# Kernel tuning notes

Measured on AMD Instinct MI355X. Metric: run time of the kernel, lower is better.

Reference implementation:

```python
import jax, jax.numpy as jnp
import numpy as np

N_NODES = 10000
N_EDGES = 80000
IN_DIM = 512
H1, H2, OUT_DIM = 4096, 1024, 7
NEG_SLOPE = 0.2


def _gat_layer(x, src, dst, W, a_src, a_dst, b, n_nodes):
    # x: [N, F_in] -> h: [N, F_out]
    h = x @ W
    # per-edge attention logits: a_src . h_i + a_dst . h_j (PyG GATConv, heads=1)
    e = jax.nn.leaky_relu((h @ a_src)[src] + (h @ a_dst)[dst], NEG_SLOPE)
    # segment softmax over destination nodes
    m = jax.ops.segment_max(e, dst, num_segments=n_nodes)
    ex = jnp.exp(e - m[dst])
    denom = jax.ops.segment_sum(ex, dst, num_segments=n_nodes)
    alpha = ex / denom[dst]
    # scatter-add weighted messages
    out = jax.ops.segment_sum(alpha[:, None] * h[src], dst, num_segments=n_nodes)
    return out + b


def setup_inputs() -> dict:
    key = jax.random.key(0)
    ks = jax.random.split(key, 16)
    s = 0.05
    inp = {
        "x": jax.random.normal(ks[0], (N_NODES, IN_DIM), dtype=jnp.float32),
        "edge_index": jax.random.randint(ks[1], (2, N_EDGES), 0, N_NODES, dtype=jnp.int32),
        "W1": jax.random.normal(ks[2], (IN_DIM, H1), dtype=jnp.float32) * s,
        "att_src1": jax.random.normal(ks[3], (H1,), dtype=jnp.float32) * s,
        "att_dst1": jax.random.normal(ks[4], (H1,), dtype=jnp.float32) * s,
        "b1": jnp.zeros((H1,), dtype=jnp.float32),
        "W2": jax.random.normal(ks[5], (H1, H2), dtype=jnp.float32) * s,
        "att_src2": jax.random.normal(ks[6], (H2,), dtype=jnp.float32) * s,
        "att_dst2": jax.random.normal(ks[7], (H2,), dtype=jnp.float32) * s,
        "b2": jnp.zeros((H2,), dtype=jnp.float32),
        "W3": jax.random.normal(ks[8], (H2, OUT_DIM), dtype=jnp.float32) * s,
        "att_src3": jax.random.normal(ks[9], (OUT_DIM,), dtype=jnp.float32) * s,
        "att_dst3": jax.random.normal(ks[10], (OUT_DIM,), dtype=jnp.float32) * s,
        "b3": jnp.zeros((OUT_DIM,), dtype=jnp.float32),
    }
    return inp


def reference(x, edge_index, W1, att_src1, att_dst1, b1,
              W2, att_src2, att_dst2, b2,
              W3, att_src3, att_dst3, b3):
    n = x.shape[0]
    loops = jnp.arange(n, dtype=edge_index.dtype)
    src = jnp.concatenate([edge_index[0], loops])  # add_self_loops=True
    dst = jnp.concatenate([edge_index[1], loops])
    h = _gat_layer(x, src, dst, W1, att_src1, att_dst1, b1, n)
    h = jax.nn.relu(h)  # dropout is identity in eval mode
    h = _gat_layer(h, src, dst, W2, att_src2, att_dst2, b2, n)
    h = jax.nn.relu(h)
    h = _gat_layer(h, src, dst, W3, att_src3, att_dst3, b3, n)
    return jax.nn.log_softmax(h, axis=1)
```

## Files before the change

kernel.cpp:

```cpp
#include <hip/hip_runtime.h>
#include <hip/hip_bf16.h>
#include <math.h>

#define NNODES  10000
#define NEDGES  80000
#define NTOT    90000
#define IN_DIM  512
#define H1_DIM  4096
#define H2_DIM  1024
#define ODIM    7
#define MAXDEG  128
#define NEG_SLOPE 0.2f

typedef __hip_bfloat16 bf16;
typedef __attribute__((ext_vector_type(8))) short short8;
typedef __attribute__((ext_vector_type(4))) float f32x4;

__device__ inline float ldf(const float* p, size_t i) { return p[i]; }
__device__ inline float ldf(const bf16* p, size_t i)  { return __bfloat162float(p[i]); }

__device__ inline void unpack_bf2(unsigned u, float& lo, float& hi) {
    union { unsigned i; float f; } a, b;
    a.i = u << 16; b.i = u & 0xffff0000u;
    lo = a.f; hi = b.f;
}

#define ASYNC_COPY16(lds, g)                                                              \
    __builtin_amdgcn_global_load_lds((const __attribute__((address_space(1))) void*)(g),  \
                                     (__attribute__((address_space(3))) void*)(lds),      \
                                     16, 0, 0)

__global__ void build_bucket(const int* __restrict__ ei, int* cnt, int* bucket) {
    int k = blockIdx.x * blockDim.x + threadIdx.x;
    if (k >= NTOT) return;
    int s, d;
    if (k < NEDGES) { s = ei[k]; d = ei[NEDGES + k]; }
    else            { s = k - NEDGES; d = s; }
    int pos = atomicAdd(&cnt[d], 1);
    if (pos < MAXDEG) bucket[d * MAXDEG + pos] = s;
}

__global__ __launch_bounds__(256) void transpose_bf16(const float* __restrict__ W,
                                                      bf16* __restrict__ WT, int R, int C) {
    __shared__ float t[32][33];
    int c0 = blockIdx.x * 32, r0 = blockIdx.y * 32;
    int x = threadIdx.x & 31, y = threadIdx.x >> 5;
    #pragma unroll
    for (int dy = 0; dy < 32; dy += 8)
        t[y + dy][x] = W[(size_t)(r0 + y + dy) * C + c0 + x];
    __syncthreads();
    #pragma unroll
    for (int dy = 0; dy < 32; dy += 8)
        WT[(size_t)(c0 + y + dy) * R + r0 + x] = __float2bfloat16(t[x][y + dy]);
}

__global__ __launch_bounds__(256) void fold_att(const float* __restrict__ W,
                                                const float* __restrict__ a_s,
                                                const float* __restrict__ a_d,
                                                float* __restrict__ w_s,
                                                float* __restrict__ w_d, int C) {
    int r = blockIdx.x;
    const float* row = W + (size_t)r * C;
    float ss = 0.f, sd = 0.f;
    for (int j = threadIdx.x; j < C; j += 256) {
        float w = row[j];
        ss = fmaf(w, a_s[j], ss);
        sd = fmaf(w, a_d[j], sd);
    }
    #pragma unroll
    for (int off = 32; off > 0; off >>= 1) {
        ss += __shfl_down(ss, off);
        sd += __shfl_down(sd, off);
    }
    __shared__ float red[2][4];
    int wave = threadIdx.x >> 6;
    if ((threadIdx.x & 63) == 0) { red[0][wave] = ss; red[1][wave] = sd; }
    __syncthreads();
    if (threadIdx.x == 0) {
        w_s[r] = red[0][0] + red[0][1] + red[0][2] + red[0][3];
        w_d[r] = red[1][0] + red[1][1] + red[1][2] + red[1][3];
    }
}

__global__ __launch_bounds__(128) void node_dots1(const float* __restrict__ X,
                                                  const float* __restrict__ w_s,
                                                  const float* __restrict__ w_d,
                                                  float* __restrict__ s_src,
                                                  float* __restrict__ s_dst) {
    int n = blockIdx.x;
    int t = threadIdx.x;
    float4 xv = ((const float4*)(X + (size_t)n * IN_DIM))[t];
    float4 wsv = ((const float4*)w_s)[t];
    float4 wdv = ((const float4*)w_d)[t];
    float ss = xv.x*wsv.x + xv.y*wsv.y + xv.z*wsv.z + xv.w*wsv.w;
    float sd = xv.x*wdv.x + xv.y*wdv.y + xv.z*wdv.z + xv.w*wdv.w;
    #pragma unroll
    for (int off = 32; off > 0; off >>= 1) {
        ss += __shfl_down(ss, off);
        sd += __shfl_down(sd, off);
    }
    __shared__ float red[2][2];
    int wave = t >> 6;
    if ((t & 63) == 0) { red[0][wave] = ss; red[1][wave] = sd; }
    __syncthreads();
    if (t == 0) {
        s_src[n] = red[0][0] + red[0][1];
        s_dst[n] = red[1][0] + red[1][1];
    }
}

__global__ __launch_bounds__(128) void agg1(const float* __restrict__ X,
                                            const float* __restrict__ s_src,
                                            const float* __restrict__ s_dst,
                                            const int* __restrict__ bucket,
                                            const int* __restrict__ cnt,
                                            bf16* __restrict__ OUT) {
    int n = blockIdx.x;
    int c = min(cnt[n], MAXDEG);
    __shared__ float alpha[MAXDEG];
    __shared__ int   ssrc[MAXDEG];
    if (threadIdx.x < c) {
        int s = bucket[n * MAXDEG + threadIdx.x];
        ssrc[threadIdx.x] = s;
        float e = s_src[s] + s_dst[n];
        alpha[threadIdx.x] = (e > 0.f) ? e : NEG_SLOPE * e;
    }
    __syncthreads();
    if (threadIdx.x == 0) {
        float m = -1e30f;
        for (int j = 0; j < c; ++j) m = fmaxf(m, alpha[j]);
        float s = 0.f;
        for (int j = 0; j < c; ++j) { float ex = __expf(alpha[j] - m); alpha[j] = ex; s += ex; }
        float inv = 1.f / s;
        for (int j = 0; j < c; ++j) alpha[j] *= inv;
    }
    __syncthreads();
    int t = threadIdx.x;
    float4 acc = {0.f, 0.f, 0.f, 0.f};
    for (int j = 0; j < c; ++j) {
        float a = alpha[j];
        float4 v = ((const float4*)(X + (size_t)ssrc[j] * IN_DIM))[t];
        acc.x = fmaf(a, v.x, acc.x); acc.y = fmaf(a, v.y, acc.y);
        acc.z = fmaf(a, v.z, acc.z); acc.w = fmaf(a, v.w, acc.w);
    }
    bf16 o[4] = { __float2bfloat16(acc.x), __float2bfloat16(acc.y),
                  __float2bfloat16(acc.z), __float2bfloat16(acc.w) };
    *(uint2*)(OUT + (size_t)n * IN_DIM + 4 * t) = *(uint2*)o;
}

__global__ __launch_bounds__(128) void agg2(const bf16* __restrict__ H,
                                            const float* __restrict__ s_src,
                                            const float* __restrict__ s_dst,
                                            const int* __restrict__ bucket,
                                            const int* __restrict__ cnt,
                                            const float* __restrict__ bias,
                                            bf16* __restrict__ OUT) {
    int n = blockIdx.x;
    int c = min(cnt[n], MAXDEG);
    __shared__ float alpha[MAXDEG];
    __shared__ int   ssrc[MAXDEG];
    if (threadIdx.x < c) {
        int s = bucket[n * MAXDEG + threadIdx.x];
        ssrc[threadIdx.x] = s;
        float e = s_src[s] + s_dst[n];
        alpha[threadIdx.x] = (e > 0.f) ? e : NEG_SLOPE * e;
    }
    __syncthreads();
    if (threadIdx.x == 0) {
        float m = -1e30f;
        for (int j = 0; j < c; ++j) m = fmaxf(m, alpha[j]);
        float s = 0.f;
        for (int j = 0; j < c; ++j) { float ex = __expf(alpha[j] - m); alpha[j] = ex; s += ex; }
        float inv = 1.f / s;
        for (int j = 0; j < c; ++j) alpha[j] *= inv;
    }
    __syncthreads();
    int t = threadIdx.x;
    float acc[8] = {};
    for (int j = 0; j < c; ++j) {
        float a = alpha[j];
        uint4 raw = ((const uint4*)(H + (size_t)ssrc[j] * H2_DIM))[t];
        float f0, f1, f2, f3, f4, f5, f6, f7;
        unpack_bf2(raw.x, f0, f1); unpack_bf2(raw.y, f2, f3);
        unpack_bf2(raw.z, f4, f5); unpack_bf2(raw.w, f6, f7);
        acc[0] = fmaf(a, f0, acc[0]); acc[1] = fmaf(a, f1, acc[1]);
        acc[2] = fmaf(a, f2, acc[2]); acc[3] = fmaf(a, f3, acc[3]);
        acc[4] = fmaf(a, f4, acc[4]); acc[5] = fmaf(a, f5, acc[5]);
        acc[6] = fmaf(a, f6, acc[6]); acc[7] = fmaf(a, f7, acc[7]);
    }
    bf16 o[8];
    #pragma unroll
    for (int k = 0; k < 8; ++k)
        o[k] = __float2bfloat16(fmaxf(acc[k] + bias[8 * t + k], 0.f));
    *(uint4*)(OUT + (size_t)n * H2_DIM + 8 * t) = *(uint4*)o;
}

template<int TN, bool BIASRELU, bool FUSEDOTS>
__global__ __launch_bounds__(256) void gemm_mfma(const bf16* __restrict__ A,
                                                 const bf16* __restrict__ BT,
                                                 const float* __restrict__ bias,
                                                 const float* __restrict__ w_s,
                                                 const float* __restrict__ w_d,
                                                 float* __restrict__ s_src,
                                                 float* __restrict__ s_dst,
                                                 bf16* __restrict__ C,
                                                 int M, int N, int K) {
    constexpr int NJ = TN / 32;
    __shared__ alignas(16) bf16 As[2][128][32];
    __shared__ alignas(16) bf16 Bs[2][TN][32];
    const int tid  = threadIdx.x;
    const int wave = tid >> 6;
    const int lane = tid & 63;
    const int row0 = blockIdx.y * 128;
    const int col0 = blockIdx.x * TN;
    const int wr0  = (wave >> 1) * 64;
    const int wc0  = (wave & 1) * (TN / 2);

    const int srow  = tid >> 2;
    const int skoff = (tid & 3) * 8;
    const bf16* agA0 = A + (size_t)min(row0 + srow,      M - 1) * K + skoff;
    const bf16* agA1 = A + (size_t)min(row0 + 64 + srow, M - 1) * K + skoff;
    const bf16* bg0  = BT + (size_t)(col0 + srow) * K + skoff;
    const bf16* bg1  = BT + (size_t)(col0 + (TN == 128 ? 64 : 0) + srow) * K + skoff;

    f32x4 acc[4][NJ] = {};

    const int fRow  = lane & 15;
    const int fKoff = (lane >> 4) * 8;

    for (int k0 = 0; k0 < K; k0 += 64) {
        #pragma unroll
        for (int h = 0; h < 2; ++h) {
            ASYNC_COPY16(&As[h][wave * 16][0],      agA0 + h * 32);
            ASYNC_COPY16(&As[h][64 + wave * 16][0], agA1 + h * 32);
            ASYNC_COPY16(&Bs[h][wave * 16][0],      bg0 + h * 32);
            if constexpr (TN == 128)
                ASYNC_COPY16(&Bs[h][(TN / 2) + wave * 16][0], bg1 + h * 32);
        }
        agA0 += 64; agA1 += 64; bg0 += 64;
        if constexpr (TN == 128) bg1 += 64;
        __syncthreads();
        #pragma unroll
        for (int h = 0; h < 2; ++h) {
            short8 af[4], bfr[NJ];
            #pragma unroll
            for (int i = 0; i < 4; ++i)
                af[i] = *(const short8*)&As[h][wr0 + i * 16 + fRow][fKoff];
            #pragma unroll
            for (int j = 0; j < NJ; ++j)
                bfr[j] = *(const short8*)&Bs[h][wc0 + j * 16 + fRow][fKoff];
            #pragma unroll
            for (int i = 0; i < 4; ++i)
                #pragma unroll
                for (int j = 0; j < NJ; ++j)
                    acc[i][j] = __builtin_amdgcn_mfma_f32_16x16x32_bf16(af[i], bfr[j], acc[i][j], 0, 0, 0);
        }
        __syncthreads();
    }

    const int crow = (lane >> 4) * 4;
    const int ccol = lane & 15;
    #pragma unroll
    for (int i = 0; i < 4; ++i) {
        #pragma unroll
        for (int r = 0; r < 4; ++r) {
            int gm = row0 + wr0 + i * 16 + crow + r;
            float vss = 0.f, vsd = 0.f;
            if (gm < M) {
                #pragma unroll
                for (int j = 0; j < NJ; ++j) {
                    int gn = col0 + wc0 + j * 16 + ccol;
                    float v = acc[i][j][r];
                    if (BIASRELU) v = fmaxf(v + bias[gn], 0.f);
                    C[(size_t)gm * N + gn] = __float2bfloat16(v);
                    if (FUSEDOTS) {
                        vss = fmaf(v, w_s[gn], vss);
                        vsd = fmaf(v, w_d[gn], vsd);
                    }
                }
            }
            if (FUSEDOTS) {
                #pragma unroll
                for (int m2 = 1; m2 < 16; m2 <<= 1) {
                    vss += __shfl_xor(vss, m2, 16);
                    vsd += __shfl_xor(vsd, m2, 16);
                }
                if ((lane & 15) == 0 && gm < M) {
                    atomicAdd(&s_src[gm], vss);
                    atomicAdd(&s_dst[gm], vsd);
                }
            }
        }
    }
}

__global__ __launch_bounds__(128) void layer3_proj(const bf16* __restrict__ X,
                                                   const float* __restrict__ W,
                                                   const float* __restrict__ a_src,
                                                   const float* __restrict__ a_dst,
                                                   float* __restrict__ H3,
                                                   float* __restrict__ s_src,
                                                   float* __restrict__ s_dst) {
    int n = blockIdx.x;
    int t = threadIdx.x;
    uint4 raw = ((const uint4*)(X + (size_t)n * H2_DIM))[t];
    float xv[8];
    unpack_bf2(raw.x, xv[0], xv[1]); unpack_bf2(raw.y, xv[2], xv[3]);
    unpack_bf2(raw.z, xv[4], xv[5]); unpack_bf2(raw.w, xv[6], xv[7]);
    float acc[ODIM] = {};
    #pragma unroll
    for (int e = 0; e < 8; ++e) {
        const float* wrow = W + (size_t)(8 * t + e) * ODIM;
        #pragma unroll
        for (int o = 0; o < ODIM; ++o)
            acc[o] = fmaf(xv[e], wrow[o], acc[o]);
    }
    #pragma unroll
    for (int o = 0; o < ODIM; ++o)
        #pragma unroll
        for (int off = 32; off > 0; off >>= 1)
            acc[o] += __shfl_down(acc[o], off);
    __shared__ float red[2][ODIM];
    int wave = t >> 6;
    if ((t & 63) == 0)
        #pragma unroll
        for (int o = 0; o < ODIM; ++o) red[wave][o] = acc[o];
    __syncthreads();
    if (t == 0) {
        float ss = 0.f, sd = 0.f;
        #pragma unroll
        for (int o = 0; o < ODIM; ++o) {
            float v = red[0][o] + red[1][o];
            H3[n * ODIM + o] = v;
            ss = fmaf(v, a_src[o], ss);
            sd = fmaf(v, a_dst[o], sd);
        }
        s_src[n] = ss; s_dst[n] = sd;
    }
}

__global__ __launch_bounds__(128) void aggregate3(const float* __restrict__ H3,
                                                  const float* __restrict__ s_src,
                                                  const float* __restrict__ s_dst,
                                                  const int* __restrict__ bucket,
                                                  const int* __restrict__ cnt,
                                                  const float* __restrict__ b3,
                                                  float* __restrict__ out) {
    int n = blockIdx.x;
    int c = min(cnt[n], MAXDEG);
    __shared__ float alpha[MAXDEG];
    __shared__ int   ssrc[MAXDEG];
    __shared__ float o[ODIM];
    if (threadIdx.x < c) {
        int s = bucket[n * MAXDEG + threadIdx.x];
        ssrc[threadIdx.x] = s;
        float e = s_src[s] + s_dst[n];
        alpha[threadIdx.x] = (e > 0.f) ? e : NEG_SLOPE * e;
    }
    __syncthreads();
    if (threadIdx.x == 0) {
        float m = -1e30f;
        for (int j = 0; j < c; ++j) m = fmaxf(m, alpha[j]);
        float s = 0.f;
        for (int j = 0; j < c; ++j) { float ex = __expf(alpha[j] - m); alpha[j] = ex; s += ex; }
        float inv = 1.f / s;
        for (int j = 0; j < c; ++j) alpha[j] *= inv;
    }
    __syncthreads();
    if (threadIdx.x < ODIM) {
        float acc = 0.f;
        for (int j = 0; j < c; ++j)
            acc = fmaf(alpha[j], H3[ssrc[j] * ODIM + threadIdx.x], acc);
        o[threadIdx.x] = acc + b3[threadIdx.x];
    }
    __syncthreads();
    if (threadIdx.x == 0) {
        float m = o[0];
        for (int k = 1; k < ODIM; ++k) m = fmaxf(m, o[k]);
        float s = 0.f;
        for (int k = 0; k < ODIM; ++k) s += __expf(o[k] - m);
        float lse = m + logf(s);
        for (int k = 0; k < ODIM; ++k) out[n * ODIM + k] = o[k] - lse;
    }
}

extern "C" void kernel_launch(void* const* d_in, const int* in_sizes, int n_in,
                              void* d_out, int out_size, void* d_ws, size_t ws_size,
                              hipStream_t stream) {
    const float* x   = (const float*)d_in[0];
    const int*   ei  = (const int*)  d_in[1];
    const float* W1  = (const float*)d_in[2];
    const float* as1 = (const float*)d_in[3];
    const float* ad1 = (const float*)d_in[4];
    const float* b1  = (const float*)d_in[5];
    const float* W2  = (const float*)d_in[6];
    const float* as2 = (const float*)d_in[7];
    const float* ad2 = (const float*)d_in[8];
    const float* b2  = (const float*)d_in[9];
    const float* W3  = (const float*)d_in[10];
    const float* as3 = (const float*)d_in[11];
    const float* ad3 = (const float*)d_in[12];
    const float* b3  = (const float*)d_in[13];
    float* outp = (float*)d_out;

    char* p = (char*)d_ws;
    bf16*  x2     = (bf16*)p;   p += (size_t)NNODES * H1_DIM * sizeof(bf16);
    bf16*  r2     = (bf16*)p;   p += (size_t)NNODES * H2_DIM * sizeof(bf16);
    bf16*  r3     = (bf16*)p;   p += (size_t)NNODES * H2_DIM * sizeof(bf16);
    bf16*  W2T    = (bf16*)p;   p += (size_t)H2_DIM * H1_DIM * sizeof(bf16);
    float* h3     = (float*)p;  p += (size_t)NNODES * ODIM * sizeof(float);
    float* ssrc   = (float*)p;  p += NNODES * sizeof(float);
    float* sdst   = (float*)p;  p += NNODES * sizeof(float);
    float* w1s    = (float*)p;  p += IN_DIM * sizeof(float);
    float* w1d    = (float*)p;  p += IN_DIM * sizeof(float);
    float* w2s    = (float*)p;  p += H1_DIM * sizeof(float);
    float* w2d    = (float*)p;  p += H1_DIM * sizeof(float);
    int*   cnt    = (int*)p;    p += NNODES * sizeof(int);
    int*   bucket = (int*)p;    p += (size_t)NNODES * MAXDEG * sizeof(int);
    size_t required = (size_t)(p - (char*)d_ws);
    if (ws_size < required) return;

    bf16* aggxb = r2;
    bf16* h2    = r2;
    bf16* W1T   = r3;
    bf16* x3    = r3;

    hipMemsetAsync(cnt, 0, NNODES * sizeof(int), stream);
    build_bucket<<<(NTOT + 255) / 256, 256, 0, stream>>>(ei, cnt, bucket);

    fold_att<<<IN_DIM, 256, 0, stream>>>(W1, as1, ad1, w1s, w1d, H1_DIM);
    node_dots1<<<NNODES, 128, 0, stream>>>(x, w1s, w1d, ssrc, sdst);
    agg1<<<NNODES, 128, 0, stream>>>(x, ssrc, sdst, bucket, cnt, aggxb);

    fold_att<<<H1_DIM, 256, 0, stream>>>(W2, as2, ad2, w2s, w2d, H2_DIM);
    hipMemsetAsync(ssrc, 0, 2 * NNODES * sizeof(float), stream);
    {
        dim3 tg(H1_DIM / 32, IN_DIM / 32);
        transpose_bf16<<<tg, 256, 0, stream>>>(W1, W1T, IN_DIM, H1_DIM);
        dim3 g(H1_DIM / 128, (NNODES + 127) / 128);
        gemm_mfma<128, true, true><<<g, 256, 0, stream>>>(aggxb, W1T, b1, w2s, w2d,
                                                          ssrc, sdst, x2, NNODES, H1_DIM, IN_DIM);
    }

    {
        dim3 tg(H2_DIM / 32, H1_DIM / 32);
        transpose_bf16<<<tg, 256, 0, stream>>>(W2, W2T, H1_DIM, H2_DIM);
        dim3 g(H2_DIM / 64, (NNODES + 127) / 128);
        gemm_mfma<64, false, false><<<g, 256, 0, stream>>>(x2, W2T, nullptr, nullptr, nullptr,
                                                           nullptr, nullptr, h2, NNODES, H2_DIM, H1_DIM);
    }
    agg2<<<NNODES, 128, 0, stream>>>(h2, ssrc, sdst, bucket, cnt, b2, x3);

    layer3_proj<<<NNODES, 128, 0, stream>>>(x3, W3, as3, ad3, h3, ssrc, sdst);
    aggregate3<<<NNODES, 128, 0, stream>>>(h3, ssrc, sdst, bucket, cnt, b3, outp);
}
```

Measured before the change: 461.2 us.

## Gather bf16 features in agg1, swizzle GEMM LDS, fold layer-3 attention into agg2

Adds a pass that converts the input features to bf16 so the layer-1 gather in agg1 reads half the bytes per neighbor. It XOR-swizzles the GEMM shared-memory k offsets to reduce LDS bank conflicts. It also folds W3 with the layer-3 attention vectors up front and computes the layer-3 source/destination scores inside agg2, which removes that work from layer3_proj. The cost is an extra conversion kernel and bf16 rounding of the raw inputs before aggregation.

```diff
diff --git a/kernel.cpp b/kernel.cpp
--- a/kernel.cpp
+++ b/kernel.cpp
@@ -16,9 +16,6 @@
 typedef __attribute__((ext_vector_type(8))) short short8;
 typedef __attribute__((ext_vector_type(4))) float f32x4;
 
-__device__ inline float ldf(const float* p, size_t i) { return p[i]; }
-__device__ inline float ldf(const bf16* p, size_t i)  { return __bfloat162float(p[i]); }
-
 __device__ inline void unpack_bf2(unsigned u, float& lo, float& hi) {
     union { unsigned i; float f; } a, b;
     a.i = u << 16; b.i = u & 0xffff0000u;
@@ -38,6 +35,16 @@
     else            { s = k - NEDGES; d = s; }
     int pos = atomicAdd(&cnt[d], 1);
     if (pos < MAXDEG) bucket[d * MAXDEG + pos] = s;
+}
+
+__global__ __launch_bounds__(256) void cvt_bf16(const float* __restrict__ X,
+                                                bf16* __restrict__ XB, size_t n4) {
+    size_t i = (size_t)blockIdx.x * blockDim.x + threadIdx.x;
+    if (i >= n4) return;
+    float4 v = ((const float4*)X)[i];
+    bf16 o[4] = { __float2bfloat16(v.x), __float2bfloat16(v.y),
+                  __float2bfloat16(v.z), __float2bfloat16(v.w) };
+    *(uint2*)(XB + 4 * i) = *(uint2*)o;
 }
 
 __global__ __launch_bounds__(256) void transpose_bf16(const float* __restrict__ W,
@@ -82,6 +89,23 @@
     }
 }
 
+__global__ __launch_bounds__(256) void fold_att3(const float* __restrict__ W3,
+                                                 const float* __restrict__ a_s,
+                                                 const float* __restrict__ a_d,
+                                                 float* __restrict__ w_s,
+                                                 float* __restrict__ w_d) {
+    int k = blockIdx.x * blockDim.x + threadIdx.x;
+    if (k >= H2_DIM) return;
+    float ss = 0.f, sd = 0.f;
+    #pragma unroll
+    for (int o = 0; o < ODIM; ++o) {
+        float w = W3[k * ODIM + o];
+        ss = fmaf(w, a_s[o], ss);
+        sd = fmaf(w, a_d[o], sd);
+    }
+    w_s[k] = ss; w_d[k] = sd;
+}
+
 __global__ __launch_bounds__(128) void node_dots1(const float* __restrict__ X,
                                                   const float* __restrict__ w_s,
                                                   const float* __restrict__ w_d,
@@ -109,7 +133,7 @@
     }
 }
 
-__global__ __launch_bounds__(128) void agg1(const float* __restrict__ X,
+__global__ __launch_bounds__(128) void agg1(const bf16* __restrict__ XB,
                                             const float* __restrict__ s_src,
                                             const float* __restrict__ s_dst,
                                             const int* __restrict__ bucket,
@@ -136,15 +160,17 @@
     }
     __syncthreads();
     int t = threadIdx.x;
-    float4 acc = {0.f, 0.f, 0.f, 0.f};
+    float acc[4] = {};
     for (int j = 0; j < c; ++j) {
         float a = alpha[j];
-        float4 v = ((const float4*)(X + (size_t)ssrc[j] * IN_DIM))[t];
-        acc.x = fmaf(a, v.x, acc.x); acc.y = fmaf(a, v.y, acc.y);
-        acc.z = fmaf(a, v.z, acc.z); acc.w = fmaf(a, v.w, acc.w);
-    }
-    bf16 o[4] = { __float2bfloat16(acc.x), __float2bfloat16(acc.y),
-                  __float2bfloat16(acc.z), __float2bfloat16(acc.w) };
+        uint2 raw = ((const uint2*)(XB + (size_t)ssrc[j] * IN_DIM))[t];
+        float f0, f1, f2, f3;
+        unpack_bf2(raw.x, f0, f1); unpack_bf2(raw.y, f2, f3);
+        acc[0] = fmaf(a, f0, acc[0]); acc[1] = fmaf(a, f1, acc[1]);
+        acc[2] = fmaf(a, f2, acc[2]); acc[3] = fmaf(a, f3, acc[3]);
+    }
+    bf16 o[4] = { __float2bfloat16(acc[0]), __float2bfloat16(acc[1]),
+                  __float2bfloat16(acc[2]), __float2bfloat16(acc[3]) };
     *(uint2*)(OUT + (size_t)n * IN_DIM + 4 * t) = *(uint2*)o;
 }
 
@@ -154,7 +180,11 @@
                                             const int* __restrict__ bucket,
                                             const int* __restrict__ cnt,
                                             const float* __restrict__ bias,
-                                            bf16* __restrict__ OUT) {
+                                            const float* __restrict__ w3s,
+                                            const float* __restrict__ w3d,
+                                            bf16* __restrict__ OUT,
+                                            float* __restrict__ s3_src,
+                                            float* __restrict__ s3_dst) {
     int n = blockIdx.x;
     int c = min(cnt[n], MAXDEG);
     __shared__ float alpha[MAXDEG];
@@ -189,10 +219,28 @@
         acc[6] = fmaf(a, f6, acc[6]); acc[7] = fmaf(a, f7, acc[7]);
     }
     bf16 o[8];
-    #pragma unroll
-    for (int k = 0; k < 8; ++k)
-        o[k] = __float2bfloat16(fmaxf(acc[k] + bias[8 * t + k], 0.f));
+    float ds = 0.f, dd = 0.f;
+    #pragma unroll
+    for (int k = 0; k < 8; ++k) {
+        float v = fmaxf(acc[k] + bias[8 * t + k], 0.f);
+        o[k] = __float2bfloat16(v);
+        ds = fmaf(v, w3s[8 * t + k], ds);
+        dd = fmaf(v, w3d[8 * t + k], dd);
+    }
     *(uint4*)(OUT + (size_t)n * H2_DIM + 8 * t) = *(uint4*)o;
+    #pragma unroll
+    for (int off = 32; off > 0; off >>= 1) {
+        ds += __shfl_down(ds, off);
+        dd += __shfl_down(dd, off);
+    }
+    __shared__ float red[2][2];
+    int wave = t >> 6;
+    if ((t & 63) == 0) { red[0][wave] = ds; red[1][wave] = dd; }
+    __syncthreads();
+    if (t == 0) {
+        s3_src[n] = red[0][0] + red[0][1];
+        s3_dst[n] = red[1][0] + red[1][1];
+    }
 }
 
 template<int TN, bool BIASRELU, bool FUSEDOTS>
@@ -217,7 +265,7 @@
     const int wc0  = (wave & 1) * (TN / 2);
 
     const int srow  = tid >> 2;
-    const int skoff = (tid & 3) * 8;
+    const int skoff = ((tid & 3) ^ (srow & 3)) * 8;
     const bf16* agA0 = A + (size_t)min(row0 + srow,      M - 1) * K + skoff;
     const bf16* agA1 = A + (size_t)min(row0 + 64 + srow, M - 1) * K + skoff;
     const bf16* bg0  = BT + (size_t)(col0 + srow) * K + skoff;
@@ -226,7 +274,7 @@
     f32x4 acc[4][NJ] = {};
 
     const int fRow  = lane & 15;
-    const int fKoff = (lane >> 4) * 8;
+    const int fKoff = (((lane >> 4) ^ (fRow & 3))) * 8;
 
     for (int k0 = 0; k0 < K; k0 += 64) {
         #pragma unroll
@@ -296,11 +344,7 @@
 
 __global__ __launch_bounds__(128) void layer3_proj(const bf16* __restrict__ X,
                                                    const float* __restrict__ W,
-                                                   const float* __restrict__ a_src,
-                                                   const float* __restrict__ a_dst,
-                                                   float* __restrict__ H3,
-                                                   float* __restrict__ s_src,
-                                                   float* __restrict__ s_dst) {
+                                                   float* __restrict__ H3) {
     int n = blockIdx.x;
     int t = threadIdx.x;
     uint4 raw = ((const uint4*)(X + (size_t)n * H2_DIM))[t];
@@ -326,17 +370,10 @@
         #pragma unroll
         for (int o = 0; o < ODIM; ++o) red[wave][o] = acc[o];
     __syncthreads();
-    if (t == 0) {
-        float ss = 0.f, sd = 0.f;
-        #pragma unroll
-        for (int o = 0; o < ODIM; ++o) {
-            float v = red[0][o] + red[1][o];
-            H3[n * ODIM + o] = v;
-            ss = fmaf(v, a_src[o], ss);
-            sd = fmaf(v, a_dst[o], sd);
-        }
-        s_src[n] = ss; s_dst[n] = sd;
-    }
+    if (t == 0)
+        #pragma unroll
+        for (int o = 0; o < ODIM; ++o)
+            H3[n * ODIM + o] = red[0][o] + red[1][o];
 }
 
 __global__ __launch_bounds__(128) void aggregate3(const float* __restrict__ H3,
@@ -411,15 +448,20 @@
     float* h3     = (float*)p;  p += (size_t)NNODES * ODIM * sizeof(float);
     float* ssrc   = (float*)p;  p += NNODES * sizeof(float);
     float* sdst   = (float*)p;  p += NNODES * sizeof(float);
+    float* ssrc3  = (float*)p;  p += NNODES * sizeof(float);
+    float* sdst3  = (float*)p;  p += NNODES * sizeof(float);
     float* w1s    = (float*)p;  p += IN_DIM * sizeof(float);
     float* w1d    = (float*)p;  p += IN_DIM * sizeof(float);
     float* w2s    = (float*)p;  p += H1_DIM * sizeof(float);
     float* w2d    = (float*)p;  p += H1_DIM * sizeof(float);
+    float* w3s    = (float*)p;  p += H2_DIM * sizeof(float);
+    float* w3d    = (float*)p;  p += H2_DIM * sizeof(float);
     int*   cnt    = (int*)p;    p += NNODES * sizeof(int);
     int*   bucket = (int*)p;    p += (size_t)NNODES * MAXDEG * sizeof(int);
     size_t required = (size_t)(p - (char*)d_ws);
     if (ws_size < required) return;
 
+    bf16* xb    = x2;
     bf16* aggxb = r2;
     bf16* h2    = r2;
     bf16* W1T   = r3;
@@ -430,7 +472,11 @@
 
     fold_att<<<IN_DIM, 256, 0, stream>>>(W1, as1, ad1, w1s, w1d, H1_DIM);
     node_dots1<<<NNODES, 128, 0, stream>>>(x, w1s, w1d, ssrc, sdst);
-    agg1<<<NNODES, 128, 0, stream>>>(x, ssrc, sdst, bucket, cnt, aggxb);
+    {
+        size_t n4 = (size_t)NNODES * IN_DIM / 4;
+        cvt_bf16<<<(unsigned)((n4 + 255) / 256), 256, 0, stream>>>(x, xb, n4);
+    }
+    agg1<<<NNODES, 128, 0, stream>>>(xb, ssrc, sdst, bucket, cnt, aggxb);
 
     fold_att<<<H1_DIM, 256, 0, stream>>>(W2, as2, ad2, w2s, w2d, H2_DIM);
     hipMemsetAsync(ssrc, 0, 2 * NNODES * sizeof(float), stream);
@@ -442,6 +488,7 @@
                                                           ssrc, sdst, x2, NNODES, H1_DIM, IN_DIM);
     }
 
+    fold_att3<<<(H2_DIM + 255) / 256, 256, 0, stream>>>(W3, as3, ad3, w3s, w3d);
     {
         dim3 tg(H2_DIM / 32, H1_DIM / 32);
         transpose_bf16<<<tg, 256, 0, stream>>>(W2, W2T, H1_DIM, H2_DIM);
@@ -449,8 +496,8 @@
         gemm_mfma<64, false, false><<<g, 256, 0, stream>>>(x2, W2T, nullptr, nullptr, nullptr,
                                                            nullptr, nullptr, h2, NNODES, H2_DIM, H1_DIM);
     }
-    agg2<<<NNODES, 128, 0, stream>>>(h2, ssrc, sdst, bucket, cnt, b2, x3);
-
-    layer3_proj<<<NNODES, 128, 0, stream>>>(x3, W3, as3, ad3, h3, ssrc, sdst);
-    aggregate3<<<NNODES, 128, 0, stream>>>(h3, ssrc, sdst, bucket, cnt, b3, outp);
-}
+    agg2<<<NNODES, 128, 0, stream>>>(h2, ssrc, sdst, bucket, cnt, b2, w3s, w3d, x3, ssrc3, sdst3);
+
+    layer3_proj<<<NNODES, 128, 0, stream>>>(x3, W3, h3);
+    aggregate3<<<NNODES, 128, 0, stream>>>(h3, ssrc3, sdst3, bucket, cnt, b3, outp);
+}
```

After: 460.8 us. About the same (-0.1%).

## Fuse layer-3 projection into agg2, gather bf16 features, swizzle GEMM LDS

Applied to the files above, without the earlier changes.

Several independent changes. The node-dot kernel now also writes a bf16 copy of x, so agg1 gathers half as many bytes per neighbour. The layer-3 projection and its attention dots are folded into agg2, which removes the x3 round trip and one launch. The MFMA GEMM gains an XOR swizzle on its LDS k-offset to reduce bank conflicts, and GEMM2 moves to 64x64 tiles for more blocks. The bf16 gather lowers precision of layer-1 inputs, and smaller tiles reduce data reuse in GEMM2.

```diff
diff --git a/kernel.cpp b/kernel.cpp
--- a/kernel.cpp
+++ b/kernel.cpp
@@ -15,9 +15,6 @@
 typedef __hip_bfloat16 bf16;
 typedef __attribute__((ext_vector_type(8))) short short8;
 typedef __attribute__((ext_vector_type(4))) float f32x4;
-
-__device__ inline float ldf(const float* p, size_t i) { return p[i]; }
-__device__ inline float ldf(const bf16* p, size_t i)  { return __bfloat162float(p[i]); }
 
 __device__ inline void unpack_bf2(unsigned u, float& lo, float& hi) {
     union { unsigned i; float f; } a, b;
@@ -82,16 +79,20 @@
     }
 }
 
-__global__ __launch_bounds__(128) void node_dots1(const float* __restrict__ X,
-                                                  const float* __restrict__ w_s,
-                                                  const float* __restrict__ w_d,
-                                                  float* __restrict__ s_src,
-                                                  float* __restrict__ s_dst) {
+__global__ __launch_bounds__(128) void dots_cvt1(const float* __restrict__ X,
+                                                 const float* __restrict__ w_s,
+                                                 const float* __restrict__ w_d,
+                                                 float* __restrict__ s_src,
+                                                 float* __restrict__ s_dst,
+                                                 bf16* __restrict__ XB) {
     int n = blockIdx.x;
     int t = threadIdx.x;
     float4 xv = ((const float4*)(X + (size_t)n * IN_DIM))[t];
     float4 wsv = ((const float4*)w_s)[t];
     float4 wdv = ((const float4*)w_d)[t];
+    bf16 o[4] = { __float2bfloat16(xv.x), __float2bfloat16(xv.y),
+                  __float2bfloat16(xv.z), __float2bfloat16(xv.w) };
+    *(uint2*)(XB + (size_t)n * IN_DIM + 4 * t) = *(uint2*)o;
     float ss = xv.x*wsv.x + xv.y*wsv.y + xv.z*wsv.z + xv.w*wsv.w;
     float sd = xv.x*wdv.x + xv.y*wdv.y + xv.z*wdv.z + xv.w*wdv.w;
     #pragma unroll
@@ -109,7 +110,7 @@
     }
 }
 
-__global__ __launch_bounds__(128) void agg1(const float* __restrict__ X,
+__global__ __launch_bounds__(128) void agg1(const bf16* __restrict__ XB,
                                             const float* __restrict__ s_src,
                                             const float* __restrict__ s_dst,
                                             const int* __restrict__ bucket,
@@ -136,25 +137,32 @@
     }
     __syncthreads();
     int t = threadIdx.x;
-    float4 acc = {0.f, 0.f, 0.f, 0.f};
+    float acc[4] = {};
     for (int j = 0; j < c; ++j) {
         float a = alpha[j];
-        float4 v = ((const float4*)(X + (size_t)ssrc[j] * IN_DIM))[t];
-        acc.x = fmaf(a, v.x, acc.x); acc.y = fmaf(a, v.y, acc.y);
-        acc.z = fmaf(a, v.z, acc.z); acc.w = fmaf(a, v.w, acc.w);
-    }
-    bf16 o[4] = { __float2bfloat16(acc.x), __float2bfloat16(acc.y),
-                  __float2bfloat16(acc.z), __float2bfloat16(acc.w) };
+        uint2 raw = ((const uint2*)(XB + (size_t)ssrc[j] * IN_DIM))[t];
+        float f0, f1, f2, f3;
+        unpack_bf2(raw.x, f0, f1); unpack_bf2(raw.y, f2, f3);
+        acc[0] = fmaf(a, f0, acc[0]); acc[1] = fmaf(a, f1, acc[1]);
+        acc[2] = fmaf(a, f2, acc[2]); acc[3] = fmaf(a, f3, acc[3]);
+    }
+    bf16 o[4] = { __float2bfloat16(acc[0]), __float2bfloat16(acc[1]),
+                  __float2bfloat16(acc[2]), __float2bfloat16(acc[3]) };
     *(uint2*)(OUT + (size_t)n * IN_DIM + 4 * t) = *(uint2*)o;
 }
 
-__global__ __launch_bounds__(128) void agg2(const bf16* __restrict__ H,
-                                            const float* __restrict__ s_src,
-                                            const float* __restrict__ s_dst,
-                                            const int* __restrict__ bucket,
-                                            const int* __restrict__ cnt,
-                                            const float* __restrict__ bias,
-                                            bf16* __restrict__ OUT) {
+__global__ __launch_bounds__(128) void agg2_h3(const bf16* __restrict__ H,
+                                               const float* __restrict__ s_src,
+                                               const float* __restrict__ s_dst,
+                                               const int* __restrict__ bucket,
+                                               const int* __restrict__ cnt,
+                                               const float* __restrict__ bias,
+                                               const float* __restrict__ W3,
+                                               const float* __restrict__ as3,
+                                               const float* __restrict__ ad3,
+                                               float* __restrict__ H3,
+                                               float* __restrict__ s3_src,
+                                               float* __restrict__ s3_dst) {
     int n = blockIdx.x;
     int c = min(cnt[n], MAXDEG);
     __shared__ float alpha[MAXDEG];
@@ -188,14 +196,40 @@
         acc[4] = fmaf(a, f4, acc[4]); acc[5] = fmaf(a, f5, acc[5]);
         acc[6] = fmaf(a, f6, acc[6]); acc[7] = fmaf(a, f7, acc[7]);
     }
-    bf16 o[8];
-    #pragma unroll
-    for (int k = 0; k < 8; ++k)
-        o[k] = __float2bfloat16(fmaxf(acc[k] + bias[8 * t + k], 0.f));
-    *(uint4*)(OUT + (size_t)n * H2_DIM + 8 * t) = *(uint4*)o;
-}
-
-template<int TN, bool BIASRELU, bool FUSEDOTS>
+    float p[ODIM] = {};
+    #pragma unroll
+    for (int k = 0; k < 8; ++k) {
+        float v = fmaxf(acc[k] + bias[8 * t + k], 0.f);
+        const float* wrow = W3 + (size_t)(8 * t + k) * ODIM;
+        #pragma unroll
+        for (int o = 0; o < ODIM; ++o)
+            p[o] = fmaf(v, wrow[o], p[o]);
+    }
+    #pragma unroll
+    for (int o = 0; o < ODIM; ++o)
+        #pragma unroll
+        for (int off = 32; off > 0; off >>= 1)
+            p[o] += __shfl_down(p[o], off);
+    __shared__ float red[2][ODIM];
+    int wave = t >> 6;
+    if ((t & 63) == 0)
+        #pragma unroll
+        for (int o = 0; o < ODIM; ++o) red[wave][o] = p[o];
+    __syncthreads();
+    if (t == 0) {
+        float ss = 0.f, sd = 0.f;
+        #pragma unroll
+        for (int o = 0; o < ODIM; ++o) {
+            float v = red[0][o] + red[1][o];
+            H3[n * ODIM + o] = v;
+            ss = fmaf(v, as3[o], ss);
+            sd = fmaf(v, ad3[o], sd);
+        }
+        s3_src[n] = ss; s3_dst[n] = sd;
+    }
+}
+
+template<int TM, int TN, bool BIASRELU, bool FUSEDOTS>
 __global__ __launch_bounds__(256) void gemm_mfma(const bf16* __restrict__ A,
                                                  const bf16* __restrict__ BT,
                                                  const float* __restrict__ bias,
@@ -205,52 +239,55 @@
                                                  float* __restrict__ s_dst,
                                                  bf16* __restrict__ C,
                                                  int M, int N, int K) {
+    constexpr int NI = TM / 32;
     constexpr int NJ = TN / 32;
-    __shared__ alignas(16) bf16 As[2][128][32];
+    __shared__ alignas(16) bf16 As[2][TM][32];
     __shared__ alignas(16) bf16 Bs[2][TN][32];
     const int tid  = threadIdx.x;
     const int wave = tid >> 6;
     const int lane = tid & 63;
-    const int row0 = blockIdx.y * 128;
+    const int row0 = blockIdx.y * TM;
     const int col0 = blockIdx.x * TN;
-    const int wr0  = (wave >> 1) * 64;
+    const int wr0  = (wave >> 1) * (TM / 2);
     const int wc0  = (wave & 1) * (TN / 2);
 
     const int srow  = tid >> 2;
-    const int skoff = (tid & 3) * 8;
-    const bf16* agA0 = A + (size_t)min(row0 + srow,      M - 1) * K + skoff;
-    const bf16* agA1 = A + (size_t)min(row0 + 64 + srow, M - 1) * K + skoff;
+    const int skoff = ((tid & 3) ^ (srow & 3)) * 8;
+    const bf16* agA0 = A + (size_t)min(row0 + srow, M - 1) * K + skoff;
+    const bf16* agA1 = (TM == 128) ? A + (size_t)min(row0 + 64 + srow, M - 1) * K + skoff : nullptr;
     const bf16* bg0  = BT + (size_t)(col0 + srow) * K + skoff;
-    const bf16* bg1  = BT + (size_t)(col0 + (TN == 128 ? 64 : 0) + srow) * K + skoff;
-
-    f32x4 acc[4][NJ] = {};
+    const bf16* bg1  = (TN == 128) ? BT + (size_t)(col0 + 64 + srow) * K + skoff : nullptr;
+
+    f32x4 acc[NI][NJ] = {};
 
     const int fRow  = lane & 15;
-    const int fKoff = (lane >> 4) * 8;
+    const int fKoff = (((lane >> 4) ^ (fRow & 3))) * 8;
 
     for (int k0 = 0; k0 < K; k0 += 64) {
         #pragma unroll
         for (int h = 0; h < 2; ++h) {
-            ASYNC_COPY16(&As[h][wave * 16][0],      agA0 + h * 32);
-            ASYNC_COPY16(&As[h][64 + wave * 16][0], agA1 + h * 32);
-            ASYNC_COPY16(&Bs[h][wave * 16][0],      bg0 + h * 32);
+            ASYNC_COPY16(&As[h][wave * 16][0], agA0 + h * 32);
+            if constexpr (TM == 128)
+                ASYNC_COPY16(&As[h][64 + wave * 16][0], agA1 + h * 32);
+            ASYNC_COPY16(&Bs[h][wave * 16][0], bg0 + h * 32);
             if constexpr (TN == 128)
-                ASYNC_COPY16(&Bs[h][(TN / 2) + wave * 16][0], bg1 + h * 32);
+                ASYNC_COPY16(&Bs[h][64 + wave * 16][0], bg1 + h * 32);
         }
-        agA0 += 64; agA1 += 64; bg0 += 64;
+        agA0 += 64; bg0 += 64;
+        if constexpr (TM == 128) agA1 += 64;
         if constexpr (TN == 128) bg1 += 64;
         __syncthreads();
         #pragma unroll
         for (int h = 0; h < 2; ++h) {
-            short8 af[4], bfr[NJ];
+            short8 af[NI], bfr[NJ];
             #pragma unroll
-            for (int i = 0; i < 4; ++i)
+            for (int i = 0; i < NI; ++i)
                 af[i] = *(const short8*)&As[h][wr0 + i * 16 + fRow][fKoff];
             #pragma unroll
             for (int j = 0; j < NJ; ++j)
                 bfr[j] = *(const short8*)&Bs[h][wc0 + j * 16 + fRow][fKoff];
             #pragma unroll
-            for (int i = 0; i < 4; ++i)
+            for (int i = 0; i < NI; ++i)
                 #pragma unroll
                 for (int j = 0; j < NJ; ++j)
                     acc[i][j] = __builtin_amdgcn_mfma_f32_16x16x32_bf16(af[i], bfr[j], acc[i][j], 0, 0, 0);
@@ -261,7 +298,7 @@
     const int crow = (lane >> 4) * 4;
     const int ccol = lane & 15;
     #pragma unroll
-    for (int i = 0; i < 4; ++i) {
+    for (int i = 0; i < NI; ++i) {
         #pragma unroll
         for (int r = 0; r < 4; ++r) {
             int gm = row0 + wr0 + i * 16 + crow + r;
@@ -294,51 +331,6 @@
     }
 }
 
-__global__ __launch_bounds__(128) void layer3_proj(const bf16* __restrict__ X,
-                                                   const float* __restrict__ W,
-                                                   const float* __restrict__ a_src,
-                                                   const float* __restrict__ a_dst,
-                                                   float* __restrict__ H3,
-                                                   float* __restrict__ s_src,
-                                                   float* __restrict__ s_dst) {
-    int n = blockIdx.x;
-    int t = threadIdx.x;
-    uint4 raw = ((const uint4*)(X + (size_t)n * H2_DIM))[t];
-    float xv[8];
-    unpack_bf2(raw.x, xv[0], xv[1]); unpack_bf2(raw.y, xv[2], xv[3]);
-    unpack_bf2(raw.z, xv[4], xv[5]); unpack_bf2(raw.w, xv[6], xv[7]);
-    float acc[ODIM] = {};
-    #pragma unroll
-    for (int e = 0; e < 8; ++e) {
-        const float* wrow = W + (size_t)(8 * t + e) * ODIM;
-        #pragma unroll
-        for (int o = 0; o < ODIM; ++o)
-            acc[o] = fmaf(xv[e], wrow[o], acc[o]);
-    }
-    #pragma unroll
-    for (int o = 0; o < ODIM; ++o)
-        #pragma unroll
-        for (int off = 32; off > 0; off >>= 1)
-            acc[o] += __shfl_down(acc[o], off);
-    __shared__ float red[2][ODIM];
-    int wave = t >> 6;
-    if ((t & 63) == 0)
-        #pragma unroll
-        for (int o = 0; o < ODIM; ++o) red[wave][o] = acc[o];
-    __syncthreads();
-    if (t == 0) {
-        float ss = 0.f, sd = 0.f;
-        #pragma unroll
-        for (int o = 0; o < ODIM; ++o) {
-            float v = red[0][o] + red[1][o];
-            H3[n * ODIM + o] = v;
-            ss = fmaf(v, a_src[o], ss);
-            sd = fmaf(v, a_dst[o], sd);
-        }
-        s_src[n] = ss; s_dst[n] = sd;
-    }
-}
-
 __global__ __launch_bounds__(128) void aggregate3(const float* __restrict__ H3,
                                                   const float* __restrict__ s_src,
                                                   const float* __restrict__ s_dst,
@@ -411,6 +403,8 @@
     float* h3     = (float*)p;  p += (size_t)NNODES * ODIM * sizeof(float);
     float* ssrc   = (float*)p;  p += NNODES * sizeof(float);
     float* sdst   = (float*)p;  p += NNODES * sizeof(float);
+    float* ssrc3  = (float*)p;  p += NNODES * sizeof(float);
+    float* sdst3  = (float*)p;  p += NNODES * sizeof(float);
     float* w1s    = (float*)p;  p += IN_DIM * sizeof(float);
     float* w1d    = (float*)p;  p += IN_DIM * sizeof(float);
     float* w2s    = (float*)p;  p += H1_DIM * sizeof(float);
@@ -420,17 +414,17 @@
     size_t required = (size_t)(p - (char*)d_ws);
     if (ws_size < required) return;
 
+    bf16* xb    = x2;
     bf16* aggxb = r2;
     bf16* h2    = r2;
     bf16* W1T   = r3;
-    bf16* x3    = r3;
 
     hipMemsetAsync(cnt, 0, NNODES * sizeof(int), stream);
     build_bucket<<<(NTOT + 255) / 256, 256, 0, stream>>>(ei, cnt, bucket);
 
     fold_att<<<IN_DIM, 256, 0, stream>>>(W1, as1, ad1, w1s, w1d, H1_DIM);
-    node_dots1<<<NNODES, 128, 0, stream>>>(x, w1s, w1d, ssrc, sdst);
-    agg1<<<NNODES, 128, 0, stream>>>(x, ssrc, sdst, bucket, cnt, aggxb);
+    dots_cvt1<<<NNODES, 128, 0, stream>>>(x, w1s, w1d, ssrc, sdst, xb);
+    agg1<<<NNODES, 128, 0, stream>>>(xb, ssrc, sdst, bucket, cnt, aggxb);
 
     fold_att<<<H1_DIM, 256, 0, stream>>>(W2, as2, ad2, w2s, w2d, H2_DIM);
     hipMemsetAsync(ssrc, 0, 2 * NNODES * sizeof(float), stream);
@@ -438,19 +432,20 @@
         dim3 tg(H1_DIM / 32, IN_DIM / 32);
         transpose_bf16<<<tg, 256, 0, stream>>>(W1, W1T, IN_DIM, H1_DIM);
         dim3 g(H1_DIM / 128, (NNODES + 127) / 128);
-        gemm_mfma<128, true, true><<<g, 256, 0, stream>>>(aggxb, W1T, b1, w2s, w2d,
-                                                          ssrc, sdst, x2, NNODES, H1_DIM, IN_DIM);
+        gemm_mfma<128, 128, true, true><<<g, 256, 0, stream>>>(aggxb, W1T, b1, w2s, w2d,
+                                                               ssrc, sdst, x2, NNODES, H1_DIM, IN_DIM);
     }
 
     {
         dim3 tg(H2_DIM / 32, H1_DIM / 32);
         transpose_bf16<<<tg, 256, 0, stream>>>(W2, W2T, H1_DIM, H2_DIM);
-        dim3 g(H2_DIM / 64, (NNODES + 127) / 128);
-        gemm_mfma<64, false, false><<<g, 256, 0, stream>>>(x2, W2T, nullptr, nullptr, nullptr,
-                                                           nullptr, nullptr, h2, NNODES, H2_DIM, H1_DIM);
-    }
-    agg2<<<NNODES, 128, 0, stream>>>(h2, ssrc, sdst, bucket, cnt, b2, x3);
-
-    layer3_proj<<<NNODES, 128, 0, stream>>>(x3, W3, as3, ad3, h3, ssrc, sdst);
-    aggregate3<<<NNODES, 128, 0, stream>>>(h3, ssrc, sdst, bucket, cnt, b3, outp);
-}
+        dim3 g(H2_DIM / 64, (NNODES + 63) / 64);
+        gemm_mfma<64, 64, false, false><<<g, 256, 0, stream>>>(x2, W2T, nullptr, nullptr, nullptr,
+                                                               nullptr, nullptr, h2, NNODES, H2_DIM, H1_DIM);
+    }
+
+    agg2_h3<<<NNODES, 128, 0, stream>>>(h2, ssrc, sdst, bucket, cnt, b2,
+                                        W3, as3, ad3, h3, ssrc3, sdst3);
+
+    aggregate3<<<NNODES, 128, 0, stream>>>(h3, ssrc3, sdst3, bucket, cnt, b3, outp);
+}
```

New measurement: 469.7 us. No clear change (+1.8%).
